# Kernel tuning notes

Hardware: AMD Instinct MI355X
Metric: run time of the kernel (lower is better)

The kernel has to match this reference:

```python
import jax, jax.numpy as jnp
import numpy as np

DN = ('NCDHW', 'OIDHW', 'NCDHW')

def conv3d(x, w, stride, padding):
    return jax.lax.conv_general_dilated(x, w, window_strides=stride, padding=padding, dimension_numbers=DN)

def swish(v):
    return v * jax.nn.sigmoid(v)

def setup_inputs() -> dict:
    key = jax.random.key(0)
    ks = jax.random.split(key, 16)
    B, Cin, Cout, E, D, H, W = 4, 64, 128, 256, 8, 128, 128
    r = lambda k, shp, s=0.05: jax.random.normal(k, shp, dtype=jnp.float32) * s
    return {
        'x': jax.random.normal(ks[0], (B, Cin, D, H, W), dtype=jnp.float32),
        'embed': jax.random.normal(ks[1], (B, E), dtype=jnp.float32),
        'context': jax.random.normal(ks[2], (B, E), dtype=jnp.float32),
        'w20': r(ks[3], (Cout, Cin, 3, 3, 3)),
        'b20': r(ks[4], (Cout,)),
        'w21': r(ks[5], (Cout, Cout, 3, 3, 3)),
        'd1_w': r(ks[6], (E, Cin)),
        'd1_b': r(ks[7], (Cin,)),
        'd2_w': r(ks[8], (E, Cout)),
        'd2_b': r(ks[9], (Cout,)),
        'res_w': r(ks[10], (Cout, Cin, 1, 1, 1)),
        'res_b': r(ks[11], (Cout,)),
        'down_w': r(ks[12], (Cout, Cout, 3, 3, 3)),
        'down_b': r(ks[13], (Cout,)),
    }

def reference(x, embed, context, w20, b20, w21, d1_w, d1_b, d2_w, d2_b, res_w, res_b, down_w, down_b):
    # --- ResBlockModulateBEST ---
    s1 = embed @ d1_w + d1_b                       # (B, Cin) time-embedding shift
    h = swish(x + s1[:, :, None, None, None])
    # dropout is identity in eval/reference mode
    h = conv3d(h, w20, (1, 1, 1), [(1, 1), (1, 1), (1, 1)]) + b20[None, :, None, None, None]
    h = swish(h)
    # modulated_conv3d: s scales the IN-channel axis of w21 per sample; since conv is
    # linear in its input channels this equals conv3d(h * s, w21) — same math, no
    # per-sample grouped conv needed.
    s2 = context @ d2_w + d2_b                     # (B, Cout == Cin of conv21)
    h = conv3d(h * s2[:, :, None, None, None], w21, (1, 1, 1), [(1, 1), (1, 1), (1, 1)])
    res = conv3d(x, res_w, (1, 1, 1), [(0, 0), (0, 0), (0, 0)]) + res_b[None, :, None, None, None]
    h = h + res
    # --- down path ---
    h = swish(h)
    out = conv3d(h, down_w, (1, 2, 2), [(1, 1), (0, 0), (0, 0)]) + down_b[None, :, None, None, None]
    return out  # (B, Cout, D, (H-3)//2+1, (W-3)//2+1) = (4,128,8,63,63)
```

## Files before the change

kernel.cpp:

```cpp
#include <hip/hip_runtime.h>
#include <cstdint>
#include <cstddef>

typedef __attribute__((ext_vector_type(8))) short bf16x8;
typedef __attribute__((ext_vector_type(4))) short bf16x4v;
typedef __attribute__((ext_vector_type(4))) float f32x4;

__device__ inline short f2bf(float f) {
  union { float f; unsigned u; } c; c.f = f;
  unsigned u = c.u;
  unsigned r = (u + 0x7fffu + ((u >> 16) & 1u)) >> 16;
  return (short)r;
}
__device__ inline float swish_f(float v) { return v / (1.f + __expf(-v)); }

__device__ inline void gld_lds16(const void* g, void* l) {
  __builtin_amdgcn_global_load_lds((const __attribute__((address_space(1))) void*)g,
                                   (__attribute__((address_space(3))) void*)l, 16, 0, 0);
}

__global__ __launch_bounds__(256) void scales_kernel(
    const float* __restrict__ embed, const float* __restrict__ context,
    const float* __restrict__ d1w, const float* __restrict__ d1b,
    const float* __restrict__ d2w, const float* __restrict__ d2b,
    float* __restrict__ s1, float* __restrict__ s2) {
  int tid = blockIdx.x * 256 + threadIdx.x;
  if (tid < 256) {
    int b = tid >> 6, c = tid & 63;
    float acc = d1b[c];
    for (int e = 0; e < 256; ++e) acc += embed[b * 256 + e] * d1w[e * 64 + c];
    s1[tid] = acc;
  } else if (tid < 768) {
    int o = tid - 256;
    int b = o >> 7, c = o & 127;
    float acc = d2b[c];
    for (int e = 0; e < 256; ++e) acc += context[b * 256 + e] * d2w[e * 128 + c];
    s2[o] = acc;
  }
}

__global__ __launch_bounds__(256) void prep_w_kernel(
    const float* __restrict__ w20, const float* __restrict__ w21,
    const float* __restrict__ wdn, const float* __restrict__ rsw,
    short* __restrict__ wt20, short* __restrict__ wt21,
    short* __restrict__ wtdn, short* __restrict__ rw) {
  for (int o = blockIdx.x * 256 + threadIdx.x; o < 1114112; o += gridDim.x * 256) {
    if (o < 221184) {
      int t = o >> 13, rem = o & 8191, co = rem >> 6, ci = rem & 63;
      wt20[o] = f2bf(w20[(co * 64 + ci) * 27 + t]);
    } else if (o < 663552) {
      int p = o - 221184;
      int t = p >> 14, rem = p & 16383, co = rem >> 7, ci = rem & 127;
      wt21[p] = f2bf(w21[(co * 128 + ci) * 27 + t]);
    } else if (o < 1105920) {
      int p = o - 663552;
      int t = p >> 14, rem = p & 16383, co = rem >> 7, ci = rem & 127;
      wtdn[p] = f2bf(wdn[(co * 128 + ci) * 27 + t]);
    } else {
      int p = o - 1105920;
      rw[p] = f2bf(rsw[p]);
    }
  }
}

__global__ __launch_bounds__(256) void prep_h1_kernel(
    const float* __restrict__ xin, const float* __restrict__ s1,
    short* __restrict__ h1) {
  __shared__ __align__(16) short sm[128 * 72];
  const int tid = threadIdx.x;
  const int gid = blockIdx.x;
  const int y = gid & 127, z = (gid >> 7) & 7, b = gid >> 10;
  const float* xbase = xin + (size_t)b * 8388608 + (size_t)z * 16384 + (size_t)y * 128;
#pragma unroll
  for (int i = 0; i < 8; ++i) {
    int e = i * 256 + tid;
    int ci = e >> 5, x4 = e & 31;
    float4 v = *(const float4*)(xbase + (size_t)ci * 131072 + x4 * 4);
    float s = s1[b * 64 + ci];
    sm[(x4 * 4 + 0) * 72 + ci] = f2bf(swish_f(v.x + s));
    sm[(x4 * 4 + 1) * 72 + ci] = f2bf(swish_f(v.y + s));
    sm[(x4 * 4 + 2) * 72 + ci] = f2bf(swish_f(v.z + s));
    sm[(x4 * 4 + 3) * 72 + ci] = f2bf(swish_f(v.w + s));
  }
  __syncthreads();
  short* orow = h1 + (size_t)gid * 8192;
#pragma unroll
  for (int i = 0; i < 4; ++i) {
    int e = i * 256 + tid;
    int xx = e >> 3, c8 = e & 7;
    *(bf16x8*)(orow + e * 8) = *(const bf16x8*)(&sm[xx * 72 + c8 * 8]);
  }
}

__global__ __launch_bounds__(256, 3) void conv20_kernel(
    const short* __restrict__ h1, const short* __restrict__ wt,
    const float* __restrict__ b20, const float* __restrict__ s2,
    short* __restrict__ h2) {
  __shared__ __align__(16) short sm[24704];
  const int tid = threadIdx.x;
  const int bi = blockIdx.x;
  const int xcd = bi & 7, slot = bi >> 3;
  const int yo = slot & 15, z = (slot >> 4) & 7, b = slot >> 7;
  const int y = xcd * 16 + yo;
  const int gid = b * 1024 + z * 128 + y;
  const int lane = tid & 63, wave = tid >> 6;
  const int wm = wave >> 1, wn = wave & 1;
  const int q = lane >> 4, n0 = lane & 15;
  const bf16x8 zz = {0, 0, 0, 0, 0, 0, 0, 0};
  short* inbuf = sm;
  f32x4 acc[4][4];
#pragma unroll
  for (int i = 0; i < 4; ++i)
#pragma unroll
    for (int j = 0; j < 4; ++j) acc[i][j] = (f32x4){0.f, 0.f, 0.f, 0.f};

  auto wstage = [&](int s) {
    const short* src = wt + (s << 13);
    short* dst = sm + 8320 + ((s & 1) << 13);
    int r = lane >> 3, ss = lane & 7;
#pragma unroll
    for (int i = 0; i < 4; ++i) {
      int c = wave * 4 + i;
      gld_lds16(src + ((c * 8 + r) << 6) + ((ss ^ r) << 3), dst + (c << 9));
    }
  };
  auto instage = [&](int it) {
    int kz = it / 3, ky = it - kz * 3;
    int zi = z + kz - 1, yi = y + ky - 1;
    if (zi >= 0 && zi < 8 && yi >= 0 && yi < 128) {
      const short* row = h1 + ((size_t)(b * 1024 + zi * 128 + yi) << 13);
#pragma unroll
      for (int i = 0; i < 4; ++i) {
        int x0 = 1 + 8 * (wave * 4 + i);
        int x = x0 + (lane >> 3);
        int c8 = (lane & 7) ^ (x & 7);
        gld_lds16(row + ((x - 1) << 6) + (c8 << 3), inbuf + (x0 << 6));
      }
    } else {
#pragma unroll
      for (int i = 0; i < 4; ++i)
        *(bf16x8*)(&inbuf[64 + (i * 256 + tid) * 8]) = zz;
    }
  };

  if (tid < 16) {
    int hf = tid >> 3, u = tid & 7;
    *(bf16x8*)(&inbuf[(hf ? 129 : 0) * 64 + u * 8]) = zz;
  }
  wstage(0);
  instage(0);
  __syncthreads();

  for (int s = 0; s < 27; ++s) {
    const int it3 = s / 3, kx = s - it3 * 3;
    if (s < 26) wstage(s + 1);
    const short* w = sm + 8320 + ((s & 1) << 13);
#pragma unroll
    for (int ch = 0; ch < 2; ++ch) {
      bf16x8 af[4], bb[4];
#pragma unroll
      for (int i = 0; i < 4; ++i)
        af[i] = *(const bf16x8*)(&w[(wm * 64 + i * 16 + n0) * 64 + (((ch * 4 + q) ^ (n0 & 7)) << 3)]);
#pragma unroll
      for (int j = 0; j < 4; ++j) {
        int xx = wn * 64 + j * 16 + n0 + kx;
        bb[j] = *(const bf16x8*)(&inbuf[xx * 64 + (((ch * 4 + q) ^ (xx & 7)) << 3)]);
      }
#pragma unroll
      for (int i = 0; i < 4; ++i)
#pragma unroll
        for (int j = 0; j < 4; ++j)
          acc[i][j] = __builtin_amdgcn_mfma_f32_16x16x32_bf16(af[i], bb[j], acc[i][j], 0, 0, 0);
    }
    __syncthreads();
    if (kx == 2 && it3 < 8) {
      instage(it3 + 1);
      __syncthreads();
    }
  }
#pragma unroll
  for (int i = 0; i < 4; ++i) {
    const int mb = wm * 64 + i * 16 + q * 4;
    const float4 bias = *(const float4*)(b20 + mb);
    const float4 sc = *(const float4*)(s2 + b * 128 + mb);
#pragma unroll
    for (int j = 0; j < 4; ++j) {
      const int n = wn * 64 + j * 16 + n0;
      bf16x4v pk;
      pk.x = f2bf(swish_f(acc[i][j][0] + bias.x) * sc.x);
      pk.y = f2bf(swish_f(acc[i][j][1] + bias.y) * sc.y);
      pk.z = f2bf(swish_f(acc[i][j][2] + bias.z) * sc.z);
      pk.w = f2bf(swish_f(acc[i][j][3] + bias.w) * sc.w);
      *(bf16x4v*)(&sm[n * 136 + mb]) = pk;
    }
  }
  __syncthreads();
  short* orow = h2 + (size_t)gid * 16384;
#pragma unroll
  for (int i = 0; i < 8; ++i) {
    int e = i * 256 + tid;
    int xx = e >> 4, c8 = e & 15;
    *(bf16x8*)(orow + e * 8) = *(const bf16x8*)(&sm[xx * 136 + c8 * 8]);
  }
}

__global__ __launch_bounds__(256, 2) void conv21_kernel(
    const short* __restrict__ h2, const short* __restrict__ wt,
    const float* __restrict__ xin, const short* __restrict__ rw,
    const float* __restrict__ res_b, short* __restrict__ h3) {
  __shared__ __align__(16) short sm[33024];
  const int tid = threadIdx.x;
  const int bi = blockIdx.x;
  const int xcd = bi & 7, slot = bi >> 3;
  const int yo = slot & 15, z = (slot >> 4) & 7, b = slot >> 7;
  const int y = xcd * 16 + yo;
  const int gid = b * 1024 + z * 128 + y;
  const int lane = tid & 63, wave = tid >> 6;
  const int wm = wave >> 1, wn = wave & 1;
  const int q = lane >> 4, n0 = lane & 15;
  const bf16x8 zz = {0, 0, 0, 0, 0, 0, 0, 0};
  short* inbuf = sm;
  f32x4 acc[4][4];
#pragma unroll
  for (int i = 0; i < 4; ++i)
#pragma unroll
    for (int j = 0; j < 4; ++j) acc[i][j] = (f32x4){0.f, 0.f, 0.f, 0.f};

  auto wstage = [&](int s) {
    int it6 = s / 6, sub = s - it6 * 6, kx = sub >> 1, ch2 = sub & 1;
    const short* src = wt + (((it6 * 3 + kx) << 14) + (ch2 << 6));
    short* dst = sm + 16640 + ((s & 1) << 13);
    int r = lane >> 3, ss = lane & 7;
#pragma unroll
    for (int i = 0; i < 4; ++i) {
      int c = wave * 4 + i;
      gld_lds16(src + ((c * 8 + r) << 7) + ((ss ^ r) << 3), dst + (c << 9));
    }
  };
  auto instage = [&](int it) {
    int kz = it / 3, ky = it - kz * 3;
    int zi = z + kz - 1, yi = y + ky - 1;
    if (zi >= 0 && zi < 8 && yi >= 0 && yi < 128) {
      const short* row = h2 + ((size_t)(b * 1024 + zi * 128 + yi) << 14);
#pragma unroll
      for (int i = 0; i < 8; ++i) {
        int x0 = 1 + 4 * (wave * 8 + i);
        int x = x0 + (lane >> 4);
        int c8 = (lane & 15) ^ (x & 15);
        gld_lds16(row + ((x - 1) << 7) + (c8 << 3), inbuf + (x0 << 7));
      }
    } else {
#pragma unroll
      for (int i = 0; i < 8; ++i)
        *(bf16x8*)(&inbuf[128 + (i * 256 + tid) * 8]) = zz;
    }
  };

  if (tid < 32) {
    int hf = tid >> 4, u = tid & 15;
    *(bf16x8*)(&inbuf[(hf ? 129 : 0) * 128 + u * 8]) = zz;
  }
  wstage(0);
  instage(0);
  __syncthreads();

  float4 xv[8];
  for (int s = 0; s < 54; ++s) {
    const int it6 = s / 6, sub = s - it6 * 6, kx = sub >> 1, ch2 = sub & 1;
    if (s < 53) wstage(s + 1);
    if (s == 51) {
      const float* xb = xin + (size_t)b * 8388608 + (size_t)z * 16384 + (size_t)y * 128;
#pragma unroll
      for (int i = 0; i < 8; ++i) {
        int e = i * 256 + tid;
        int ci = e >> 5, x4 = e & 31;
        xv[i] = *(const float4*)(xb + (size_t)ci * 131072 + x4 * 4);
      }
    }
    const short* w = sm + 16640 + ((s & 1) << 13);
#pragma unroll
    for (int chL = 0; chL < 2; ++chL) {
      const int ch = ch2 * 2 + chL;
      bf16x8 af[4], bb[4];
#pragma unroll
      for (int i = 0; i < 4; ++i)
        af[i] = *(const bf16x8*)(&w[(wm * 64 + i * 16 + n0) * 64 + (((chL * 4 + q) ^ (n0 & 7)) << 3)]);
#pragma unroll
      for (int j = 0; j < 4; ++j) {
        int xx = wn * 64 + j * 16 + n0 + kx;
        bb[j] = *(const bf16x8*)(&inbuf[(xx << 7) + (((ch * 4 + q) ^ (xx & 15)) << 3)]);
      }
#pragma unroll
      for (int i = 0; i < 4; ++i)
#pragma unroll
        for (int j = 0; j < 4; ++j)
          acc[i][j] = __builtin_amdgcn_mfma_f32_16x16x32_bf16(af[i], bb[j], acc[i][j], 0, 0, 0);
    }
    __syncthreads();
    if (sub == 5 && it6 < 8) {
      instage(it6 + 1);
      __syncthreads();
    }
  }
  short* rbuf = sm + 16640;
  {
#pragma unroll
    for (int i = 0; i < 8; ++i) {
      int e = i * 256 + tid;
      int ci = e >> 5, x4 = e & 31;
      int u0 = ci >> 3, cl = ci & 7;
#pragma unroll
      for (int k = 0; k < 4; ++k) {
        int xx = x4 * 4 + k;
        float fv = (k == 0) ? xv[i].x : (k == 1) ? xv[i].y : (k == 2) ? xv[i].z : xv[i].w;
        rbuf[xx * 64 + ((u0 ^ (xx & 7)) << 3) + cl] = f2bf(fv);
      }
    }
  }
  __syncthreads();
#pragma unroll
  for (int ch = 0; ch < 2; ++ch) {
    bf16x8 af[4], bb[4];
#pragma unroll
    for (int i = 0; i < 4; ++i)
      af[i] = *(const bf16x8*)(rw + (wm * 64 + i * 16 + n0) * 64 + ch * 32 + q * 8);
#pragma unroll
    for (int j = 0; j < 4; ++j) {
      int xx = wn * 64 + j * 16 + n0;
      bb[j] = *(const bf16x8*)(&rbuf[xx * 64 + (((ch * 4 + q) ^ (xx & 7)) << 3)]);
    }
#pragma unroll
    for (int i = 0; i < 4; ++i)
#pragma unroll
      for (int j = 0; j < 4; ++j)
        acc[i][j] = __builtin_amdgcn_mfma_f32_16x16x32_bf16(af[i], bb[j], acc[i][j], 0, 0, 0);
  }
  __syncthreads();
#pragma unroll
  for (int i = 0; i < 4; ++i) {
    const int mb = wm * 64 + i * 16 + q * 4;
    const float4 bias = *(const float4*)(res_b + mb);
#pragma unroll
    for (int j = 0; j < 4; ++j) {
      const int n = wn * 64 + j * 16 + n0;
      bf16x4v pk;
      pk.x = f2bf(swish_f(acc[i][j][0] + bias.x));
      pk.y = f2bf(swish_f(acc[i][j][1] + bias.y));
      pk.z = f2bf(swish_f(acc[i][j][2] + bias.z));
      pk.w = f2bf(swish_f(acc[i][j][3] + bias.w));
      *(bf16x4v*)(&sm[n * 136 + mb]) = pk;
    }
  }
  __syncthreads();
  short* orow = h3 + (size_t)gid * 16384;
#pragma unroll
  for (int i = 0; i < 8; ++i) {
    int e = i * 256 + tid;
    int xx = e >> 4, c8 = e & 15;
    *(bf16x8*)(orow + e * 8) = *(const bf16x8*)(&sm[xx * 136 + c8 * 8]);
  }
}

__global__ __launch_bounds__(256, 2) void down_kernel(
    const short* __restrict__ h3, const short* __restrict__ wt,
    const float* __restrict__ dnb, float* __restrict__ out) {
  __shared__ __align__(16) short sm[33024];
  const int tid = threadIdx.x;
  const int bi = blockIdx.x;
  const int o = (bi & 7) * 252 + (bi >> 3);
  const int yo = o % 63;
  const int zb = o / 63;
  const int z = zb & 7, b = zb >> 3;
  const int lane = tid & 63, wave = tid >> 6;
  const int wm = wave >> 1, wn = wave & 1;
  const int q = lane >> 4, n0 = lane & 15;
  const bf16x8 zz = {0, 0, 0, 0, 0, 0, 0, 0};
  short* inbuf = sm;
  f32x4 acc[4][2];
#pragma unroll
  for (int i = 0; i < 4; ++i)
#pragma unroll
    for (int j = 0; j < 2; ++j) acc[i][j] = (f32x4){0.f, 0.f, 0.f, 0.f};

  auto wstage = [&](int s) {
    int it6 = s / 6, sub = s - it6 * 6, kx = sub >> 1, ch2 = sub & 1;
    const short* src = wt + (((it6 * 3 + kx) << 14) + (ch2 << 6));
    short* dst = sm + 16640 + ((s & 1) << 13);
    int r = lane >> 3, ss = lane & 7;
#pragma unroll
    for (int i = 0; i < 4; ++i) {
      int c = wave * 4 + i;
      gld_lds16(src + ((c * 8 + r) << 7) + ((ss ^ r) << 3), dst + (c << 9));
    }
  };
  auto instage = [&](int it) {
    int kz = it / 3, ky = it - kz * 3;
    int zi = z + kz - 1;
    int yi = 2 * yo + ky;
    if (zi >= 0 && zi < 8) {
      const short* row = h3 + ((size_t)(b * 1024 + zi * 128 + yi) << 14);
#pragma unroll
      for (int i = 0; i < 8; ++i) {
        int x0 = 4 * (wave * 8 + i);
        int x = x0 + (lane >> 4);
        int c8 = (lane & 15) ^ (x & 15);
        gld_lds16(row + (x << 7) + (c8 << 3), inbuf + (x0 << 7));
      }
    } else {
#pragma unroll
      for (int i = 0; i < 8; ++i)
        *(bf16x8*)(&inbuf[(i * 256 + tid) * 8]) = zz;
    }
  };

  if (tid < 32) {
    int hf = tid >> 4, u = tid & 15;
    *(bf16x8*)(&inbuf[(128 + hf) * 128 + u * 8]) = zz;
  }
  wstage(0);
  instage(0);
  __syncthreads();

  for (int s = 0; s < 54; ++s) {
    const int it6 = s / 6, sub = s - it6 * 6, kx = sub >> 1, ch2 = sub & 1;
    if (s < 53) wstage(s + 1);
    const short* w = sm + 16640 + ((s & 1) << 13);
#pragma unroll
    for (int chL = 0; chL < 2; ++chL) {
      const int ch = ch2 * 2 + chL;
      bf16x8 af[4], bb[2];
#pragma unroll
      for (int i = 0; i < 4; ++i)
        af[i] = *(const bf16x8*)(&w[(wm * 64 + i * 16 + n0) * 64 + (((chL * 4 + q) ^ (n0 & 7)) << 3)]);
#pragma unroll
      for (int j = 0; j < 2; ++j) {
        int xp = 2 * (wn * 32 + j * 16 + n0) + kx;
        bb[j] = *(const bf16x8*)(&inbuf[(xp << 7) + (((ch * 4 + q) ^ (xp & 15)) << 3)]);
      }
#pragma unroll
      for (int i = 0; i < 4; ++i)
#pragma unroll
        for (int j = 0; j < 2; ++j)
          acc[i][j] = __builtin_amdgcn_mfma_f32_16x16x32_bf16(af[i], bb[j], acc[i][j], 0, 0, 0);
    }
    __syncthreads();
    if (sub == 5 && it6 < 8) {
      instage(it6 + 1);
      __syncthreads();
    }
  }
  float* fsm = (float*)sm;
#pragma unroll
  for (int i = 0; i < 4; ++i) {
    const int mb = wm * 64 + i * 16 + q * 4;
    const float4 bias = *(const float4*)(dnb + mb);
#pragma unroll
    for (int j = 0; j < 2; ++j) {
      const int n = wn * 32 + j * 16 + n0;
      f32x4 v;
      v[0] = acc[i][j][0] + bias.x;
      v[1] = acc[i][j][1] + bias.y;
      v[2] = acc[i][j][2] + bias.z;
      v[3] = acc[i][j][3] + bias.w;
      *(f32x4*)(&fsm[n * 132 + mb]) = v;
    }
  }
  __syncthreads();
#pragma unroll
  for (int it = 0; it < 32; ++it) {
    int idx = it * 256 + tid;
    int co = idx >> 6, xl = idx & 63;
    if (xl < 63)
      out[((size_t)(b * 128 + co) * 8 + z) * 3969 + yo * 63 + xl] = fsm[xl * 132 + co];
  }
}

extern "C" void kernel_launch(void* const* d_in, const int* in_sizes, int n_in,
                              void* d_out, int out_size, void* d_ws, size_t ws_size,
                              hipStream_t stream) {
  const float* x       = (const float*)d_in[0];
  const float* embed   = (const float*)d_in[1];
  const float* context = (const float*)d_in[2];
  const float* w20     = (const float*)d_in[3];
  const float* b20     = (const float*)d_in[4];
  const float* w21     = (const float*)d_in[5];
  const float* d1w     = (const float*)d_in[6];
  const float* d1b     = (const float*)d_in[7];
  const float* d2w     = (const float*)d_in[8];
  const float* d2b     = (const float*)d_in[9];
  const float* resw    = (const float*)d_in[10];
  const float* resb    = (const float*)d_in[11];
  const float* dnw     = (const float*)d_in[12];
  const float* dnb     = (const float*)d_in[13];
  float* out = (float*)d_out;
  char* ws = (char*)d_ws;
  float* s1   = (float*)(ws + 0);
  float* s2   = (float*)(ws + 1024);
  short* wt20 = (short*)(ws + 4096);
  short* wt21 = (short*)(ws + 446464);
  short* wtdn = (short*)(ws + 1331200);
  short* rw   = (short*)(ws + 2215936);
  short* h1   = (short*)(ws + 2232320);
  short* h2   = (short*)(ws + 69341184);
  short* h3   = (short*)(ws + 203558912);

  scales_kernel<<<3, 256, 0, stream>>>(embed, context, d1w, d1b, d2w, d2b, s1, s2);
  prep_w_kernel<<<1088, 256, 0, stream>>>(w20, w21, dnw, resw, wt20, wt21, wtdn, rw);
  prep_h1_kernel<<<4096, 256, 0, stream>>>(x, s1, h1);
  conv20_kernel<<<4096, 256, 0, stream>>>(h1, wt20, b20, s2, h2);
  conv21_kernel<<<4096, 256, 0, stream>>>(h2, wt21, x, rw, resb, h3);
  down_kernel<<<2016, 256, 0, stream>>>(h3, wtdn, dnb, out);
}
```

Baseline: 1.091 ms.

## Replace __syncthreads with partial vmcnt waits and split acquire/release barriers

Each of the three conv main loops now uses explicit s_waitcnt vmcnt(N) plus s_barrier in place of __syncthreads, which drains all outstanding loads. The acquire step waits only for the previous stage's async global-to-LDS loads and leaves the just-issued next weight stage in flight. The extra barrier after input staging is removed. The intent is to keep prefetches overlapping with MFMA work. The risk is correctness: the hard-coded vmcnt counts must match the number of loads issued, including the x prefetch around s==51.

```diff
diff --git a/kernel.cpp b/kernel.cpp
--- a/kernel.cpp
+++ b/kernel.cpp
@@ -18,6 +18,16 @@
   __builtin_amdgcn_global_load_lds((const __attribute__((address_space(1))) void*)g,
                                    (__attribute__((address_space(3))) void*)l, 16, 0, 0);
 }
+
+#define ACQ(VM) do {                                                     \
+    asm volatile("s_waitcnt vmcnt(" VM ")" ::: "memory");                \
+    __builtin_amdgcn_s_barrier();                                        \
+    asm volatile("" ::: "memory");                                       \
+  } while (0)
+#define REL() do {                                                       \
+    asm volatile("" ::: "memory");                                       \
+    __builtin_amdgcn_s_barrier();                                        \
+  } while (0)
 
 __global__ __launch_bounds__(256) void scales_kernel(
     const float* __restrict__ embed, const float* __restrict__ context,
@@ -140,6 +150,7 @@
 #pragma unroll
       for (int i = 0; i < 4; ++i)
         *(bf16x8*)(&inbuf[64 + (i * 256 + tid) * 8]) = zz;
+      asm volatile("s_waitcnt lgkmcnt(0)" ::: "memory");
     }
   };
 
@@ -154,6 +165,7 @@
   for (int s = 0; s < 27; ++s) {
     const int it3 = s / 3, kx = s - it3 * 3;
     if (s < 26) wstage(s + 1);
+    if (s < 26) ACQ("4"); else ACQ("0");
     const short* w = sm + 8320 + ((s & 1) << 13);
 #pragma unroll
     for (int ch = 0; ch < 2; ++ch) {
@@ -172,11 +184,8 @@
         for (int j = 0; j < 4; ++j)
           acc[i][j] = __builtin_amdgcn_mfma_f32_16x16x32_bf16(af[i], bb[j], acc[i][j], 0, 0, 0);
     }
-    __syncthreads();
-    if (kx == 2 && it3 < 8) {
-      instage(it3 + 1);
-      __syncthreads();
-    }
+    REL();
+    if (kx == 2 && it3 < 8) instage(it3 + 1);
   }
 #pragma unroll
   for (int i = 0; i < 4; ++i) {
@@ -253,6 +262,7 @@
 #pragma unroll
       for (int i = 0; i < 8; ++i)
         *(bf16x8*)(&inbuf[128 + (i * 256 + tid) * 8]) = zz;
+      asm volatile("s_waitcnt lgkmcnt(0)" ::: "memory");
     }
   };
 
@@ -268,6 +278,9 @@
   for (int s = 0; s < 54; ++s) {
     const int it6 = s / 6, sub = s - it6 * 6, kx = sub >> 1, ch2 = sub & 1;
     if (s < 53) wstage(s + 1);
+    if (s == 52)      ACQ("12");
+    else if (s == 53) ACQ("0");
+    else              ACQ("4");
     if (s == 51) {
       const float* xb = xin + (size_t)b * 8388608 + (size_t)z * 16384 + (size_t)y * 128;
 #pragma unroll
@@ -296,11 +309,8 @@
         for (int j = 0; j < 4; ++j)
           acc[i][j] = __builtin_amdgcn_mfma_f32_16x16x32_bf16(af[i], bb[j], acc[i][j], 0, 0, 0);
     }
-    __syncthreads();
-    if (sub == 5 && it6 < 8) {
-      instage(it6 + 1);
-      __syncthreads();
-    }
+    REL();
+    if (sub == 5 && it6 < 8) instage(it6 + 1);
   }
   short* rbuf = sm + 16640;
   {
@@ -410,6 +420,7 @@
 #pragma unroll
       for (int i = 0; i < 8; ++i)
         *(bf16x8*)(&inbuf[(i * 256 + tid) * 8]) = zz;
+      asm volatile("s_waitcnt lgkmcnt(0)" ::: "memory");
     }
   };
 
@@ -424,6 +435,7 @@
   for (int s = 0; s < 54; ++s) {
     const int it6 = s / 6, sub = s - it6 * 6, kx = sub >> 1, ch2 = sub & 1;
     if (s < 53) wstage(s + 1);
+    if (s < 53) ACQ("4"); else ACQ("0");
     const short* w = sm + 16640 + ((s & 1) << 13);
 #pragma unroll
     for (int chL = 0; chL < 2; ++chL) {
@@ -443,11 +455,8 @@
         for (int j = 0; j < 2; ++j)
           acc[i][j] = __builtin_amdgcn_mfma_f32_16x16x32_bf16(af[i], bb[j], acc[i][j], 0, 0, 0);
     }
-    __syncthreads();
-    if (sub == 5 && it6 < 8) {
-      instage(it6 + 1);
-      __syncthreads();
-    }
+    REL();
+    if (sub == 5 && it6 < 8) instage(it6 + 1);
   }
   float* fsm = (float*)sm;
 #pragma unroll
```

Measured after the change: 1.055 ms. 1.03x faster.
